# Performance work log

Hardware: AMD Instinct MI355X
Metric: run time of the kernel (lower is better)

Reference implementation:

```python
import jax, jax.numpy as jnp
import numpy as np

ALPHA = 0.929
BETA = 15.99
TAU = 0.0
EPS = 1e-8


def setup_inputs() -> dict:
    key = jax.random.key(0)
    k1, k2 = jax.random.split(key)
    head_outputs = jax.random.normal(k1, (8, 2048, 16, 128), dtype=jnp.float32)
    G = jax.random.normal(k2, (16, 16), dtype=jnp.float32)
    return {"head_outputs": head_outputs, "G": G}


def reference(head_outputs, G):
    B, T, H, d_h = head_outputs.shape
    N = B * T
    outputs = head_outputs.reshape(N, H, d_h)
    mu = outputs.mean(axis=0, keepdims=True)
    # torch .std() is unbiased (ddof=1)
    sigma = outputs.std(axis=0, keepdims=True, ddof=1)
    O_tilde = (outputs - mu) / (sigma + EPS)  # (N, H, d_h)

    # All pairwise cross-correlations in one batched contraction: (H, H, d_h, d_h)
    C = jnp.einsum('nid,nje->ijde', O_tilde, O_tilde) / N
    diff = C - jnp.eye(d_h, dtype=C.dtype)  # subtract_identity=True
    pair_loss = jnp.sum(diff * diff, axis=(2, 3))  # (H, H)

    w = ALPHA + (1.0 - ALPHA) * jax.nn.softplus(-BETA * (G - TAU))  # (H, H)

    upper = jnp.triu(jnp.ones((H, H), dtype=C.dtype), k=1)  # i < j mask
    n_pairs = H * (H - 1) // 2
    loss = jnp.sum(upper * w * pair_loss) / n_pairs
    return loss
```

## Files before the change

kernel.cpp:

```cpp
#include <hip/hip_runtime.h>
#include <hip/hip_bf16.h>

#define N_TOK   16384
#define HDIM    2048
#define NH      16
#define DH      128
#define NPAIRS  120
#define KCHUNKS 4
#define NKT     (N_TOK / 64)
#define KT_PER_CHUNK (NKT / KCHUNKS)
#define SKT     KT_PER_CHUNK
#define PANEL_BYTES 8192

#define SUM_OFF    0u
#define SUMSQ_OFF  8192u
#define PC_OFF     36864u
#define XT_OFF     31494144u

typedef float f32x4  __attribute__((ext_vector_type(4)));
typedef float f32x16 __attribute__((ext_vector_type(16)));
typedef int   v8i    __attribute__((ext_vector_type(8)));
typedef int   v2i    __attribute__((ext_vector_type(2)));
typedef long long i64t;

#if __has_builtin(__builtin_amdgcn_cvt_pk_fp8_f32)
__device__ __forceinline__ unsigned pk4_fp8(float a, float b, float c, float d) {
    int w = __builtin_amdgcn_cvt_pk_fp8_f32(a, b, 0, false);
    w = __builtin_amdgcn_cvt_pk_fp8_f32(c, d, w, true);
    return (unsigned)w;
}
#else
__device__ __forceinline__ unsigned char f2e4m3_sw(float f) {
    unsigned u = __float_as_uint(f);
    unsigned s = (u >> 24) & 0x80u;
    unsigned a = u & 0x7fffffffu;
    if (a >= 0x43e00000u) return (unsigned char)(s | 0x7eu);
    if (a < 0x3c800000u) {
        float av = __uint_as_float(a);
        int q = (int)rintf(av * 512.0f);
        return (unsigned char)(s | (unsigned)q);
    }
    unsigned lsb = (a >> 20) & 1u;
    a += 0x7ffffu + lsb;
    int e8 = (int)(a >> 23) - 120;
    unsigned m = (a >> 20) & 7u;
    return (unsigned char)(s | ((unsigned)e8 << 3) | m);
}
__device__ __forceinline__ unsigned pk4_fp8(float a, float b, float c, float d) {
    return (unsigned)f2e4m3_sw(a) | ((unsigned)f2e4m3_sw(b) << 8) |
           ((unsigned)f2e4m3_sw(c) << 16) | ((unsigned)f2e4m3_sw(d) << 24);
}
#endif

__global__ __launch_bounds__(256)
void stats_transpose_kernel(const float* __restrict__ X,
                            float* __restrict__ sum, float* __restrict__ sumsq,
                            unsigned char* __restrict__ Xt) {
    __shared__ float tile[64][129];
    __shared__ float sred[4][32][8];
    const int h  = blockIdx.x;
    const int by = blockIdx.y;
    const int n0 = by * 64;
    const int tx = threadIdx.x;
    const int w  = tx >> 6, l = tx & 63;
    const int cq = tx & 31;
    const int rq0 = tx >> 5;

    float4 s  = make_float4(0.f, 0.f, 0.f, 0.f);
    float4 ss = make_float4(0.f, 0.f, 0.f, 0.f);
    #pragma unroll
    for (int it = 0; it < 8; ++it) {
        int r = it * 8 + rq0;
        float4 x = *(const float4*)(X + (size_t)(n0 + r) * HDIM + h * DH + cq * 4);
        s.x += x.x; s.y += x.y; s.z += x.z; s.w += x.w;
        ss.x += x.x * x.x; ss.y += x.y * x.y; ss.z += x.z * x.z; ss.w += x.w * x.w;
        tile[r][cq * 4 + 0] = x.x; tile[r][cq * 4 + 1] = x.y;
        tile[r][cq * 4 + 2] = x.z; tile[r][cq * 4 + 3] = x.w;
    }
    s.x += __shfl_down(s.x, 32);  s.y += __shfl_down(s.y, 32);
    s.z += __shfl_down(s.z, 32);  s.w += __shfl_down(s.w, 32);
    ss.x += __shfl_down(ss.x, 32); ss.y += __shfl_down(ss.y, 32);
    ss.z += __shfl_down(ss.z, 32); ss.w += __shfl_down(ss.w, 32);
    if (l < 32) {
        sred[w][l][0] = s.x;  sred[w][l][1] = s.y;
        sred[w][l][2] = s.z;  sred[w][l][3] = s.w;
        sred[w][l][4] = ss.x; sred[w][l][5] = ss.y;
        sred[w][l][6] = ss.z; sred[w][l][7] = ss.w;
    }
    __syncthreads();
    if (tx < 32) {
        float a0 = 0.f, a1 = 0.f, a2 = 0.f, a3 = 0.f;
        float b0 = 0.f, b1 = 0.f, b2 = 0.f, b3 = 0.f;
        #pragma unroll
        for (int w2 = 0; w2 < 4; ++w2) {
            a0 += sred[w2][tx][0]; a1 += sred[w2][tx][1];
            a2 += sred[w2][tx][2]; a3 += sred[w2][tx][3];
            b0 += sred[w2][tx][4]; b1 += sred[w2][tx][5];
            b2 += sred[w2][tx][6]; b3 += sred[w2][tx][7];
        }
        int c = h * DH + tx * 4;
        atomicAdd(&sum[c + 0], a0);  atomicAdd(&sum[c + 1], a1);
        atomicAdd(&sum[c + 2], a2);  atomicAdd(&sum[c + 3], a3);
        atomicAdd(&sumsq[c + 0], b0); atomicAdd(&sumsq[c + 1], b1);
        atomicAdd(&sumsq[c + 2], b2); atomicAdd(&sumsq[c + 3], b3);
    }
    unsigned char* panel = Xt + ((size_t)h * NKT + by) * PANEL_BYTES;
    #pragma unroll
    for (int it = 0; it < 2; ++it) {
        int q = it * 256 + tx;
        int c = q >> 2, o = q & 3;
        uint4 pk;
        pk.x = pk4_fp8(tile[o*16+ 0][c], tile[o*16+ 1][c], tile[o*16+ 2][c], tile[o*16+ 3][c]);
        pk.y = pk4_fp8(tile[o*16+ 4][c], tile[o*16+ 5][c], tile[o*16+ 6][c], tile[o*16+ 7][c]);
        pk.z = pk4_fp8(tile[o*16+ 8][c], tile[o*16+ 9][c], tile[o*16+10][c], tile[o*16+11][c]);
        pk.w = pk4_fp8(tile[o*16+12][c], tile[o*16+13][c], tile[o*16+14][c], tile[o*16+15][c]);
        uint4 outv = ((c >> 3) & 1) ? make_uint4(pk.z, pk.w, pk.x, pk.y) : pk;
        *(uint4*)(panel + c * 64 + o * 16) = outv;
    }
}

__device__ __forceinline__ void gload16(const void* gsrc, void* ldst) {
    __builtin_amdgcn_global_load_lds(
        (const __attribute__((address_space(1))) unsigned int*)gsrc,
        (__attribute__((address_space(3))) unsigned int*)ldst,
        16, 0, 0);
}

__device__ __forceinline__ v8i gather_frag(const unsigned char* rp,
                                           int o0, int o1, int o2, int o3) {
    v2i x0 = *(const v2i*)(rp + o0);
    v2i x1 = *(const v2i*)(rp + o1);
    v2i x2 = *(const v2i*)(rp + o2);
    v2i x3 = *(const v2i*)(rp + o3);
    v8i r;
    r[0] = x0[0]; r[1] = x0[1];
    r[2] = x1[0]; r[3] = x1[1];
    r[4] = x2[0]; r[5] = x2[1];
    r[6] = x3[0]; r[7] = x3[1];
    return r;
}

__global__ __launch_bounds__(512, 2)
void gram_kernel(const unsigned char* __restrict__ Xt, float* __restrict__ pairP) {
    const int kc = blockIdx.x;
    const int p  = blockIdx.y;
    int i = 0, rem = p;
    while (rem >= NH - 1 - i) { rem -= NH - 1 - i; ++i; }
    const int j = i + 1 + rem;

    __shared__ alignas(16) unsigned char lds[4 * 2 * PANEL_BYTES];

    const int tx = threadIdx.x;
    const int w  = tx >> 6, l = tx & 63;
    const int wm = w >> 2, wn = w & 3;
    const int l31 = l & 31, half = l >> 5;

    unsigned int goff;
    {
        int r0 = tx >> 2, cl0 = tx & 3;
        goff = (unsigned int)(r0 * 64 + (cl0 ^ ((r0 >> 1) & 3)) * 16);
    }
    const int lo = w * 1024;
    const char* Abase = (const char*)Xt + ((size_t)i * NKT + (size_t)kc * KT_PER_CHUNK) * PANEL_BYTES;
    const char* Bbase = (const char*)Xt + ((size_t)j * NKT + (size_t)kc * KT_PER_CHUNK) * PANEL_BYTES;

    auto STAGE = [&](int s, int slot) {
        const char* pa = Abase + (size_t)s * PANEL_BYTES;
        const char* pb = Bbase + (size_t)s * PANEL_BYTES;
        char* base = (char*)lds + slot * (2 * PANEL_BYTES);
        gload16(pa + goff, base + lo);
        gload16(pb + goff, base + PANEL_BYTES + lo);
    };

    f32x16 acc0, acc1;
    #pragma unroll
    for (int e = 0; e < 16; ++e) { acc0[e] = 0.f; acc1[e] = 0.f; }

    const int usw = (l31 & 6) | ((l31 >> 3) & 1);
    const int puo0 = (((half * 4) + 0) ^ usw) * 8;
    const int puo1 = (((half * 4) + 1) ^ usw) * 8;
    const int puo2 = (((half * 4) + 2) ^ usw) * 8;
    const int puo3 = (((half * 4) + 3) ^ usw) * 8;
    const int offA0 = (wm * 64 +  0 + l31) * 64;
    const int offA1 = (wm * 64 + 32 + l31) * 64;
    const int offB  = PANEL_BYTES + (wn * 32 + l31) * 64;

    STAGE(0, 0); STAGE(1, 1); STAGE(2, 2);
    asm volatile("s_waitcnt vmcnt(4)\n\ts_barrier" ::: "memory");

    for (int s = 0; s < SKT; ++s) {
        STAGE((s + 3) & (SKT - 1), (s + 3) & 3);

        const unsigned char* sb = lds + (s & 3) * (2 * PANEL_BYTES);
        __builtin_amdgcn_s_setprio(1);
        v8i a0 = gather_frag(sb + offA0, puo0, puo1, puo2, puo3);
        v8i a1 = gather_frag(sb + offA1, puo0, puo1, puo2, puo3);
        v8i b  = gather_frag(sb + offB,  puo0, puo1, puo2, puo3);
        acc0 = __builtin_amdgcn_mfma_scale_f32_32x32x64_f8f6f4(
            a0, b, acc0, 0, 0, 0, 0x7F7F7F7F, 0, 0x7F7F7F7F);
        acc1 = __builtin_amdgcn_mfma_scale_f32_32x32x64_f8f6f4(
            a1, b, acc1, 0, 0, 0, 0x7F7F7F7F, 0, 0x7F7F7F7F);
        __builtin_amdgcn_s_setprio(0);

        asm volatile("s_waitcnt vmcnt(4) lgkmcnt(0)\n\ts_barrier" ::: "memory");
    }
    asm volatile("s_waitcnt vmcnt(0)" ::: "memory");

    float* pc = pairP + ((size_t)kc * NPAIRS + (size_t)p) * (DH * DH);
    #pragma unroll
    for (int e = 0; e < 16; ++e) {
        int rl = (e & 3) + 8 * (e >> 2) + 4 * half;
        int row = wm * 64 + rl;
        int col = wn * 32 + l31;
        pc[row * DH + col]        = acc0[e];
        pc[(row + 32) * DH + col] = acc1[e];
    }
}

__global__ void pair_reduce_kernel(const float* __restrict__ pairP, const float* __restrict__ G,
                                   const float* __restrict__ sum, const float* __restrict__ sumsq,
                                   float* __restrict__ out) {
    int p = blockIdx.x;
    int i = 0, rem = p;
    while (rem >= NH - 1 - i) { rem -= NH - 1 - i; ++i; }
    int j = i + 1 + rem;
    __shared__ float smui[DH], smuj[DH], sri[DH], srj[DH];
    {
        int t = threadIdx.x;
        int head = (t < DH) ? i : j;
        int d = t & (DH - 1);
        int c = head * DH + d;
        float m = sum[c] * (1.f / (float)N_TOK);
        float var = (sumsq[c] - (float)N_TOK * m * m) * (1.f / (float)(N_TOK - 1));
        var = fmaxf(var, 0.f);
        float r = 1.f / (sqrtf(var) + 1e-8f);
        if (t < DH) { smui[d] = m; sri[d] = r; }
        else        { smuj[d] = m; srj[d] = r; }
    }
    __syncthreads();
    const float invN = 1.f / (float)N_TOK;
    const size_t SLAB = (size_t)NPAIRS * DH * DH;
    const float* base = pairP + (size_t)p * (DH * DH);
    float s = 0.f;
    for (int q = threadIdx.x; q < (DH * DH) / 4; q += 256) {
        float4 v = ((const float4*)base)[q];
        #pragma unroll
        for (int kc = 1; kc < KCHUNKS; ++kc) {
            float4 t = ((const float4*)(base + kc * SLAB))[q];
            v.x += t.x; v.y += t.y; v.z += t.z; v.w += t.w;
        }
        int d = q >> 5;
        int e0 = (q & 31) * 4;
        float md = smui[d], rd = sri[d];
        float cn, df;
        cn = (v.x * invN - md * smuj[e0 + 0]) * rd * srj[e0 + 0];
        df = cn - ((d == e0 + 0) ? 1.f : 0.f); s += df * df;
        cn = (v.y * invN - md * smuj[e0 + 1]) * rd * srj[e0 + 1];
        df = cn - ((d == e0 + 1) ? 1.f : 0.f); s += df * df;
        cn = (v.z * invN - md * smuj[e0 + 2]) * rd * srj[e0 + 2];
        df = cn - ((d == e0 + 2) ? 1.f : 0.f); s += df * df;
        cn = (v.w * invN - md * smuj[e0 + 3]) * rd * srj[e0 + 3];
        df = cn - ((d == e0 + 3) ? 1.f : 0.f); s += df * df;
    }
    for (int o = 32; o; o >>= 1) s += __shfl_down(s, o);
    __shared__ float red[4];
    if ((threadIdx.x & 63) == 0) red[threadIdx.x >> 6] = s;
    __syncthreads();
    if (threadIdx.x == 0) {
        float t = red[0] + red[1] + red[2] + red[3];
        float x = -15.99f * (G[i * NH + j] - 0.0f);
        float sp = (x > 20.f) ? x : log1pf(expf(x));
        float wgt = 0.929f + (1.f - 0.929f) * sp;
        atomicAdd(out, wgt * t * (1.f / (float)NPAIRS));
    }
}

extern "C" void kernel_launch(void* const* d_in, const int* in_sizes, int n_in,
                              void* d_out, int out_size, void* d_ws, size_t ws_size,
                              hipStream_t stream) {
    const float* X = (const float*)d_in[0];
    const float* G = (const float*)d_in[1];
    float* out = (float*)d_out;
    char* ws = (char*)d_ws;

    float*         sum   = (float*)(ws + SUM_OFF);
    float*         sumsq = (float*)(ws + SUMSQ_OFF);
    float*         pairP = (float*)(ws + PC_OFF);
    unsigned char* Xt    = (unsigned char*)(ws + XT_OFF);

    hipMemsetAsync(ws + SUM_OFF, 0, 16384, stream);
    hipMemsetAsync(d_out, 0, 4, stream);

    stats_transpose_kernel<<<dim3(16, 256), 256, 0, stream>>>(X, sum, sumsq, Xt);
    gram_kernel<<<dim3(KCHUNKS, NPAIRS), 512, 0, stream>>>(Xt, pairP);
    pair_reduce_kernel<<<NPAIRS, 256, 0, stream>>>(pairP, G, sum, sumsq, out);
}
```

Before: 239.9 us.

## Compute two head rows per block against one column head, split K into eight chunks

The Gram kernel now groups heads into pairs (2g, 2g+1) and computes both 128x128 cross-blocks against a shared column head j in one block. The B panel is loaded once and reused across two A panels, with a 2x2 MFMA tile per wave. The K dimension is split into 8 chunks instead of 4 to raise the block count, and the pipeline goes from 4 stages to 2. This cuts global panel loads per pair. In exchange it computes some wasted tiles (hi >= j, which are discarded), doubles the partial-sum workspace and its reduction traffic, and the shallower prefetch risks exposing load latency.

```diff
diff --git a/kernel.cpp b/kernel.cpp
--- a/kernel.cpp
+++ b/kernel.cpp
@@ -6,16 +6,16 @@
 #define NH      16
 #define DH      128
 #define NPAIRS  120
-#define KCHUNKS 4
+#define KCHUNKS 8
 #define NKT     (N_TOK / 64)
 #define KT_PER_CHUNK (NKT / KCHUNKS)
-#define SKT     KT_PER_CHUNK
+#define NCOLS   64
 #define PANEL_BYTES 8192
 
 #define SUM_OFF    0u
 #define SUMSQ_OFF  8192u
 #define PC_OFF     36864u
-#define XT_OFF     31494144u
+#define XT_OFF     62951424u
 
 typedef float f32x4  __attribute__((ext_vector_type(4)));
 typedef float f32x16 __attribute__((ext_vector_type(16)));
@@ -140,19 +140,20 @@
     return r;
 }
 
-__global__ __launch_bounds__(512, 2)
+__global__ __launch_bounds__(512, 4)
 void gram_kernel(const unsigned char* __restrict__ Xt, float* __restrict__ pairP) {
-    const int kc = blockIdx.x;
-    const int p  = blockIdx.y;
-    int i = 0, rem = p;
-    while (rem >= NH - 1 - i) { rem -= NH - 1 - i; ++i; }
-    const int j = i + 1 + rem;
-
-    __shared__ alignas(16) unsigned char lds[4 * 2 * PANEL_BYTES];
+    const int bid = blockIdx.x;
+    const int kc  = bid & 7;
+    const int col = bid >> 3;
+    int g = 0, rem = col;
+    while (rem >= 15 - 2 * g) { rem -= 15 - 2 * g; ++g; }
+    const int j = 2 * g + 1 + rem;
+
+    __shared__ alignas(16) unsigned char lds[2 * 3 * PANEL_BYTES];
 
     const int tx = threadIdx.x;
     const int w  = tx >> 6, l = tx & 63;
-    const int wm = w >> 2, wn = w & 3;
+    const int wm = w >> 1, wn = w & 1;
     const int l31 = l & 31, half = l >> 5;
 
     unsigned int goff;
@@ -161,59 +162,77 @@
         goff = (unsigned int)(r0 * 64 + (cl0 ^ ((r0 >> 1) & 3)) * 16);
     }
     const int lo = w * 1024;
-    const char* Abase = (const char*)Xt + ((size_t)i * NKT + (size_t)kc * KT_PER_CHUNK) * PANEL_BYTES;
-    const char* Bbase = (const char*)Xt + ((size_t)j * NKT + (size_t)kc * KT_PER_CHUNK) * PANEL_BYTES;
-
-    auto STAGE = [&](int s, int slot) {
-        const char* pa = Abase + (size_t)s * PANEL_BYTES;
-        const char* pb = Bbase + (size_t)s * PANEL_BYTES;
-        char* base = (char*)lds + slot * (2 * PANEL_BYTES);
-        gload16(pa + goff, base + lo);
-        gload16(pb + goff, base + PANEL_BYTES + lo);
+    const char* P0 = (const char*)Xt + ((size_t)(2 * g)     * NKT + (size_t)kc * KT_PER_CHUNK) * PANEL_BYTES;
+    const char* P1 = (const char*)Xt + ((size_t)(2 * g + 1) * NKT + (size_t)kc * KT_PER_CHUNK) * PANEL_BYTES;
+    const char* PB = (const char*)Xt + ((size_t)j           * NKT + (size_t)kc * KT_PER_CHUNK) * PANEL_BYTES;
+
+    auto STAGE = [&](int s, char* base) {
+        gload16(P0 + (size_t)s * PANEL_BYTES + goff, base + lo);
+        gload16(P1 + (size_t)s * PANEL_BYTES + goff, base + PANEL_BYTES + lo);
+        gload16(PB + (size_t)s * PANEL_BYTES + goff, base + 2 * PANEL_BYTES + lo);
     };
 
-    f32x16 acc0, acc1;
+    f32x16 acc00, acc01, acc10, acc11;
     #pragma unroll
-    for (int e = 0; e < 16; ++e) { acc0[e] = 0.f; acc1[e] = 0.f; }
+    for (int e = 0; e < 16; ++e) { acc00[e] = 0.f; acc01[e] = 0.f; acc10[e] = 0.f; acc11[e] = 0.f; }
 
     const int usw = (l31 & 6) | ((l31 >> 3) & 1);
     const int puo0 = (((half * 4) + 0) ^ usw) * 8;
     const int puo1 = (((half * 4) + 1) ^ usw) * 8;
     const int puo2 = (((half * 4) + 2) ^ usw) * 8;
     const int puo3 = (((half * 4) + 3) ^ usw) * 8;
-    const int offA0 = (wm * 64 +  0 + l31) * 64;
-    const int offA1 = (wm * 64 + 32 + l31) * 64;
-    const int offB  = PANEL_BYTES + (wn * 32 + l31) * 64;
-
-    STAGE(0, 0); STAGE(1, 1); STAGE(2, 2);
-    asm volatile("s_waitcnt vmcnt(4)\n\ts_barrier" ::: "memory");
-
-    for (int s = 0; s < SKT; ++s) {
-        STAGE((s + 3) & (SKT - 1), (s + 3) & 3);
-
-        const unsigned char* sb = lds + (s & 3) * (2 * PANEL_BYTES);
+    const int offA0 = (wm >> 1) * PANEL_BYTES + ((wm & 1) * 64 +  0 + l31) * 64;
+    const int offA1 = (wm >> 1) * PANEL_BYTES + ((wm & 1) * 64 + 32 + l31) * 64;
+    const int offB0 = 2 * PANEL_BYTES + (wn * 64 +  0 + l31) * 64;
+    const int offB1 = 2 * PANEL_BYTES + (wn * 64 + 32 + l31) * 64;
+
+    STAGE(0, (char*)lds);
+    asm volatile("s_waitcnt vmcnt(0)\n\ts_barrier" ::: "memory");
+
+    int cur = 0;
+    for (int s = 0; s < KT_PER_CHUNK; ++s) {
+        if (s + 1 < KT_PER_CHUNK)
+            STAGE(s + 1, (char*)lds + (cur ^ 1) * (3 * PANEL_BYTES));
+
+        const unsigned char* base = lds + cur * (3 * PANEL_BYTES);
         __builtin_amdgcn_s_setprio(1);
-        v8i a0 = gather_frag(sb + offA0, puo0, puo1, puo2, puo3);
-        v8i a1 = gather_frag(sb + offA1, puo0, puo1, puo2, puo3);
-        v8i b  = gather_frag(sb + offB,  puo0, puo1, puo2, puo3);
-        acc0 = __builtin_amdgcn_mfma_scale_f32_32x32x64_f8f6f4(
-            a0, b, acc0, 0, 0, 0, 0x7F7F7F7F, 0, 0x7F7F7F7F);
-        acc1 = __builtin_amdgcn_mfma_scale_f32_32x32x64_f8f6f4(
-            a1, b, acc1, 0, 0, 0, 0x7F7F7F7F, 0, 0x7F7F7F7F);
+        v8i a0 = gather_frag(base + offA0, puo0, puo1, puo2, puo3);
+        v8i a1 = gather_frag(base + offA1, puo0, puo1, puo2, puo3);
+        {
+            v8i b0 = gather_frag(base + offB0, puo0, puo1, puo2, puo3);
+            acc00 = __builtin_amdgcn_mfma_scale_f32_32x32x64_f8f6f4(
+                a0, b0, acc00, 0, 0, 0, 0x7F7F7F7F, 0, 0x7F7F7F7F);
+            acc10 = __builtin_amdgcn_mfma_scale_f32_32x32x64_f8f6f4(
+                a1, b0, acc10, 0, 0, 0, 0x7F7F7F7F, 0, 0x7F7F7F7F);
+        }
+        {
+            v8i b1 = gather_frag(base + offB1, puo0, puo1, puo2, puo3);
+            acc01 = __builtin_amdgcn_mfma_scale_f32_32x32x64_f8f6f4(
+                a0, b1, acc01, 0, 0, 0, 0x7F7F7F7F, 0, 0x7F7F7F7F);
+            acc11 = __builtin_amdgcn_mfma_scale_f32_32x32x64_f8f6f4(
+                a1, b1, acc11, 0, 0, 0, 0x7F7F7F7F, 0, 0x7F7F7F7F);
+        }
         __builtin_amdgcn_s_setprio(0);
 
-        asm volatile("s_waitcnt vmcnt(4) lgkmcnt(0)\n\ts_barrier" ::: "memory");
-    }
-    asm volatile("s_waitcnt vmcnt(0)" ::: "memory");
-
-    float* pc = pairP + ((size_t)kc * NPAIRS + (size_t)p) * (DH * DH);
-    #pragma unroll
-    for (int e = 0; e < 16; ++e) {
-        int rl = (e & 3) + 8 * (e >> 2) + 4 * half;
-        int row = wm * 64 + rl;
-        int col = wn * 32 + l31;
-        pc[row * DH + col]        = acc0[e];
-        pc[(row + 32) * DH + col] = acc1[e];
+        if (s + 1 < KT_PER_CHUNK)
+            asm volatile("s_waitcnt vmcnt(0) lgkmcnt(0)\n\ts_barrier" ::: "memory");
+        cur ^= 1;
+    }
+
+    const int hi = 2 * g + (wm >> 1);
+    if (hi < j) {
+        const int p = hi * 15 - (hi * (hi - 1)) / 2 + (j - hi - 1);
+        float* pc = pairP + ((size_t)kc * NPAIRS + (size_t)p) * (DH * DH);
+        #pragma unroll
+        for (int e = 0; e < 16; ++e) {
+            int rl  = (e & 3) + 8 * (e >> 2) + 4 * half;
+            int row = (wm & 1) * 64 + rl;
+            int c0  = wn * 64 + l31;
+            pc[row * DH + c0]             = acc00[e];
+            pc[row * DH + c0 + 32]        = acc01[e];
+            pc[(row + 32) * DH + c0]      = acc10[e];
+            pc[(row + 32) * DH + c0 + 32] = acc11[e];
+        }
     }
 }
 
@@ -292,6 +311,6 @@
     hipMemsetAsync(d_out, 0, 4, stream);
 
     stats_transpose_kernel<<<dim3(16, 256), 256, 0, stream>>>(X, sum, sumsq, Xt);
-    gram_kernel<<<dim3(KCHUNKS, NPAIRS), 512, 0, stream>>>(Xt, pairP);
+    gram_kernel<<<NCOLS * KCHUNKS, 512, 0, stream>>>(Xt, pairP);
     pair_reduce_kernel<<<NPAIRS, 256, 0, stream>>>(pairP, G, sum, sumsq, out);
 }
```

Result: no change. 244.4 us (+1.8%).
